# Performance work log

Measured on AMD Instinct MI355X. Metric: run time of the kernel, lower is better.

## Reference

```python
import jax, jax.numpy as jnp
import numpy as np

N = 50000
IN_DIM = 256
HID = 64
HEADS = 4
OUT_DIM = 64
NEG_SLOPE = 0.2


def gat_conv(x, src, dst, W, att_src, att_dst, bias, heads, out_ch):
    # x: [N, F_in]; src/dst: [E] (self-loops already appended)
    n = x.shape[0]
    h = (x @ W).reshape(n, heads, out_ch)                     # [N,H,C]
    a_s = jnp.sum(h * att_src, axis=-1)                       # [N,H]
    a_d = jnp.sum(h * att_dst, axis=-1)                       # [N,H]
    e = jax.nn.leaky_relu(a_s[src] + a_d[dst], NEG_SLOPE)     # [E,H]
    # segment softmax over destination neighborhoods
    m = jax.ops.segment_max(e, dst, num_segments=n)           # [N,H]
    m = jnp.where(jnp.isfinite(m), m, 0.0)
    ex = jnp.exp(e - m[dst])                                  # [E,H]
    denom = jax.ops.segment_sum(ex, dst, num_segments=n)      # [N,H]
    alpha = ex / (denom[dst] + 1e-16)                         # [E,H]
    msg = alpha[:, :, None] * h[src]                          # [E,H,C]
    out = jax.ops.segment_sum(msg, dst, num_segments=n)       # [N,H,C]
    return out.reshape(n, heads * out_ch) + bias


def setup_inputs() -> dict:
    key = jax.random.key(0)
    ks = jax.random.split(key, 10)
    glorot = lambda k, shape: jax.random.normal(k, shape, jnp.float32) * np.sqrt(2.0 / (shape[0] + shape[-1]))
    x = jax.random.normal(ks[0], (N, IN_DIM), jnp.float32)
    edge_index = jax.random.randint(ks[1], (2, 800000), 0, N, jnp.int64)
    W1 = glorot(ks[2], (IN_DIM, HEADS * HID))
    att_src1 = glorot(ks[3], (HEADS, HID))
    att_dst1 = glorot(ks[4], (HEADS, HID))
    b1 = jnp.zeros((HEADS * HID,), jnp.float32)
    W2 = glorot(ks[5], (HEADS * HID, OUT_DIM))
    att_src2 = glorot(ks[6], (1, OUT_DIM))
    att_dst2 = glorot(ks[7], (1, OUT_DIM))
    b2 = jnp.zeros((OUT_DIM,), jnp.float32)
    return {"x": x, "edge_index": edge_index, "W1": W1, "att_src1": att_src1,
            "att_dst1": att_dst1, "b1": b1, "W2": W2, "att_src2": att_src2,
            "att_dst2": att_dst2, "b2": b2}


def reference(x, edge_index, W1, att_src1, att_dst1, b1, W2, att_src2, att_dst2, b2):
    # add self loops (PyG GATConv default)
    loops = jnp.arange(N, dtype=edge_index.dtype)
    src = jnp.concatenate([edge_index[0], loops])
    dst = jnp.concatenate([edge_index[1], loops])
    h = gat_conv(x, src, dst, W1, att_src1, att_dst1, b1, HEADS, HID)
    h = jax.nn.elu(h)
    out = gat_conv(h, src, dst, W2, att_src2, att_dst2, b2, 1, OUT_DIM)
    return out
```

## Files before the change

### kernel.cpp

```cpp
#include <hip/hip_runtime.h>
#include <math.h>

#define N_NODES 50000
#define E_RAW   800000
#define E_TOT   850000
#define NEG_SLOPE 0.2f
#define NBC 196

typedef __attribute__((ext_vector_type(8))) short short8;
typedef __attribute__((ext_vector_type(4))) float f32x4;

__device__ __forceinline__ float lrelu(float v) {
    return v >= 0.f ? v : NEG_SLOPE * v;
}
__device__ __forceinline__ unsigned short f2bf(float f) {
    union { float f; unsigned u; } v; v.f = f;
    unsigned r = v.u + 0x7FFF + ((v.u >> 16) & 1);
    return (unsigned short)(r >> 16);
}
__device__ __forceinline__ float bf2f(unsigned short h) {
    union { unsigned u; float f; } v; v.u = ((unsigned)h) << 16;
    return v.f;
}
__device__ __forceinline__ int C1(int p) { return (p & 15) * 16 + (p >> 4); }
__device__ __forceinline__ int C2(int p) { return (p & 3) * 16 + (p >> 2); }

__global__ __launch_bounds__(256) void k_hist(
    const int* __restrict__ dst, int* __restrict__ counts)
{
    int e = blockIdx.x * 256 + threadIdx.x;
    if (e >= E_TOT) return;
    int d = (e < E_RAW) ? dst[e] : e - E_RAW;
    atomicAdd(&counts[d], 1);
}

__global__ __launch_bounds__(256) void k_scan1(
    const int* __restrict__ counts, int* __restrict__ off, int* __restrict__ bsum)
{
    __shared__ int sh[256];
    int t = threadIdx.x, i = blockIdx.x * 256 + t;
    int c = (i < N_NODES) ? counts[i] : 0;
    sh[t] = c; __syncthreads();
    for (int ofs = 1; ofs < 256; ofs <<= 1) {
        int v = (t >= ofs) ? sh[t - ofs] : 0;
        __syncthreads(); sh[t] += v; __syncthreads();
    }
    if (i < N_NODES) off[i] = sh[t] - c;
    if (t == 255) bsum[blockIdx.x] = sh[255];
}

__global__ __launch_bounds__(256) void k_scan2(int* __restrict__ bsum)
{
    __shared__ int sh[256];
    int t = threadIdx.x;
    int c = (t < NBC) ? bsum[t] : 0;
    sh[t] = c; __syncthreads();
    for (int ofs = 1; ofs < 256; ofs <<= 1) {
        int v = (t >= ofs) ? sh[t - ofs] : 0;
        __syncthreads(); sh[t] += v; __syncthreads();
    }
    if (t < NBC) bsum[t] = sh[t] - c;
}

__global__ __launch_bounds__(256) void k_scan3(
    int* __restrict__ off, const int* __restrict__ bsum)
{
    int i = blockIdx.x * 256 + threadIdx.x;
    if (i < N_NODES) off[i] += bsum[blockIdx.x];
    if (i == 0) off[N_NODES] = E_TOT;
}

__global__ __launch_bounds__(256) void k_scatter(
    const int* __restrict__ src, const int* __restrict__ dst,
    const int* __restrict__ off, int* __restrict__ cursor,
    int* __restrict__ esrc)
{
    int e = blockIdx.x * 256 + threadIdx.x;
    if (e >= E_TOT) return;
    int s, d;
    if (e < E_RAW) { s = src[e]; d = dst[e]; } else { s = e - E_RAW; d = s; }
    int pos = off[d] + atomicAdd(&cursor[d], 1);
    esrc[pos] = s;
}

__global__ __launch_bounds__(256) void k_prepw1(
    const float* __restrict__ W1, unsigned short* __restrict__ Wf1)
{
    int idx = blockIdx.x * 256 + threadIdx.x;
    int lane = idx & 63, kb = (idx >> 6) & 7, nb = idx >> 9;
    int c = nb * 16 + (lane & 15);
    int k0 = kb * 32 + ((lane >> 4) & 3) * 8;
    short8 pk;
#pragma unroll
    for (int j = 0; j < 8; ++j)
        pk[j] = (short)f2bf(W1[(k0 + j) * 256 + c]);
    *(short8*)&Wf1[idx * 8] = pk;
}

__global__ __launch_bounds__(256) void k_prepw2(
    const float* __restrict__ W2, unsigned short* __restrict__ Wf2)
{
    int idx = blockIdx.x * 256 + threadIdx.x;
    int lane = idx & 63, kb = (idx >> 6) & 7, nb = idx >> 9;
    int c = nb * 16 + (lane & 15);
    int k0 = kb * 32 + ((lane >> 4) & 3) * 8;
    short8 pk;
#pragma unroll
    for (int j = 0; j < 8; ++j) {
        int ktrue = C1(k0 + j);
        pk[j] = (short)f2bf(W2[ktrue * 64 + c]);
    }
    *(short8*)&Wf2[idx * 8] = pk;
}

__global__ __launch_bounds__(256) void k_gemm1(
    const float* __restrict__ x, const unsigned short* __restrict__ Wf1,
    const float* __restrict__ att_src, const float* __restrict__ att_dst,
    unsigned short* __restrict__ h1b, float* __restrict__ as1, float* __restrict__ ad1)
{
    const int t = threadIdx.x;
    const int lane = t & 63;
    const int w = t >> 6;
    const int rbase = blockIdx.x * 16;
    const int q  = lane & 15;
    const int kg = lane >> 4;
    const int rowA = rbase + q;

    f32x4 acc[4];
#pragma unroll
    for (int nb = 0; nb < 4; ++nb) acc[nb] = (f32x4){0.f, 0.f, 0.f, 0.f};

    short8 b[2][4];
    float4 a0, a1, a0n, a1n;
    {
        const float* ap = &x[rowA * 256 + kg * 8];
        a0 = *(const float4*)ap;
        a1 = *(const float4*)(ap + 4);
#pragma unroll
        for (int nb = 0; nb < 4; ++nb)
            b[0][nb] = *(const short8*)&Wf1[(((w * 4 + nb) * 8 + 0) * 64 + lane) * 8];
    }
#pragma unroll
    for (int kb = 0; kb < 8; ++kb) {
        if (kb < 7) {
            const float* ap = &x[rowA * 256 + (kb + 1) * 32 + kg * 8];
            a0n = *(const float4*)ap;
            a1n = *(const float4*)(ap + 4);
#pragma unroll
            for (int nb = 0; nb < 4; ++nb)
                b[(kb + 1) & 1][nb] =
                    *(const short8*)&Wf1[(((w * 4 + nb) * 8 + kb + 1) * 64 + lane) * 8];
        }
        short8 af;
        af[0] = (short)f2bf(a0.x); af[1] = (short)f2bf(a0.y);
        af[2] = (short)f2bf(a0.z); af[3] = (short)f2bf(a0.w);
        af[4] = (short)f2bf(a1.x); af[5] = (short)f2bf(a1.y);
        af[6] = (short)f2bf(a1.z); af[7] = (short)f2bf(a1.w);
#pragma unroll
        for (int nb = 0; nb < 4; ++nb)
            acc[nb] = __builtin_amdgcn_mfma_f32_16x16x32_bf16(af, b[kb & 1][nb], acc[nb], 0, 0, 0);
        if (kb < 7) { a0 = a0n; a1 = a1n; }
    }

#pragma unroll
    for (int reg = 0; reg < 4; ++reg) {
        int n = rbase + kg * 4 + reg;
        ushort4 pk;
        pk.x = f2bf(acc[0][reg]); pk.y = f2bf(acc[1][reg]);
        pk.z = f2bf(acc[2][reg]); pk.w = f2bf(acc[3][reg]);
        *(ushort4*)&h1b[n * 256 + q * 16 + w * 4] = pk;
    }
    float asv[4], adv[4];
#pragma unroll
    for (int nb = 0; nb < 4; ++nb) {
        int col = (w * 4 + nb) * 16 + q;
        asv[nb] = att_src[col];
        adv[nb] = att_dst[col];
    }
#pragma unroll
    for (int reg = 0; reg < 4; ++reg) {
        float s = acc[0][reg]*asv[0] + acc[1][reg]*asv[1] + acc[2][reg]*asv[2] + acc[3][reg]*asv[3];
        float d = acc[0][reg]*adv[0] + acc[1][reg]*adv[1] + acc[2][reg]*adv[2] + acc[3][reg]*adv[3];
#pragma unroll
        for (int ofs = 1; ofs < 16; ofs <<= 1) {
            s += __shfl_xor(s, ofs);
            d += __shfl_xor(d, ofs);
        }
        if (q == 0) {
            int n = rbase + kg * 4 + reg;
            as1[n * 4 + w] = s;
            ad1[n * 4 + w] = d;
        }
    }
}

__global__ __launch_bounds__(256) void k_gather1(
    const int* __restrict__ esrc, const int* __restrict__ off,
    const float* __restrict__ as1, const float* __restrict__ ad1,
    const unsigned short* __restrict__ h1b, const float* __restrict__ b1,
    unsigned short* __restrict__ hmid)
{
    int d    = (blockIdx.x * 256 + threadIdx.x) >> 6;
    int lane = threadIdx.x & 63;
    if (d >= N_NODES) return;
    const int head = lane & 3;
    const float adv = ad1[d * 4 + head];
    const int e0 = off[d], e1 = off[d + 1];
    float4 acc = make_float4(0.f, 0.f, 0.f, 0.f);
    float dn = 0.f;
    int e = e0;
    for (; e + 3 < e1; e += 4) {
        int s0 = esrc[e], s1 = esrc[e + 1], s2 = esrc[e + 2], s3 = esrc[e + 3];
        float w0 = __expf(lrelu(as1[s0 * 4 + head] + adv));
        float w1 = __expf(lrelu(as1[s1 * 4 + head] + adv));
        float w2 = __expf(lrelu(as1[s2 * 4 + head] + adv));
        float w3 = __expf(lrelu(as1[s3 * 4 + head] + adv));
        ushort4 u0 = *(const ushort4*)&h1b[s0 * 256 + lane * 4];
        ushort4 u1 = *(const ushort4*)&h1b[s1 * 256 + lane * 4];
        ushort4 u2 = *(const ushort4*)&h1b[s2 * 256 + lane * 4];
        ushort4 u3 = *(const ushort4*)&h1b[s3 * 256 + lane * 4];
        dn += (w0 + w1) + (w2 + w3);
        acc.x = fmaf(w0, bf2f(u0.x), fmaf(w1, bf2f(u1.x), fmaf(w2, bf2f(u2.x), fmaf(w3, bf2f(u3.x), acc.x))));
        acc.y = fmaf(w0, bf2f(u0.y), fmaf(w1, bf2f(u1.y), fmaf(w2, bf2f(u2.y), fmaf(w3, bf2f(u3.y), acc.y))));
        acc.z = fmaf(w0, bf2f(u0.z), fmaf(w1, bf2f(u1.z), fmaf(w2, bf2f(u2.z), fmaf(w3, bf2f(u3.z), acc.z))));
        acc.w = fmaf(w0, bf2f(u0.w), fmaf(w1, bf2f(u1.w), fmaf(w2, bf2f(u2.w), fmaf(w3, bf2f(u3.w), acc.w))));
    }
    for (; e < e1; ++e) {
        int s0 = esrc[e];
        float w0 = __expf(lrelu(as1[s0 * 4 + head] + adv));
        ushort4 u0 = *(const ushort4*)&h1b[s0 * 256 + lane * 4];
        dn += w0;
        acc.x = fmaf(w0, bf2f(u0.x), acc.x);
        acc.y = fmaf(w0, bf2f(u0.y), acc.y);
        acc.z = fmaf(w0, bf2f(u0.z), acc.z);
        acc.w = fmaf(w0, bf2f(u0.w), acc.w);
    }
    const float inv = 1.f / (dn + 1e-16f);
    float o[4] = {acc.x, acc.y, acc.z, acc.w};
    ushort4 pk;
    unsigned short* pko = (unsigned short*)&pk;
#pragma unroll
    for (int i = 0; i < 4; ++i) {
        float v = o[i] * inv + b1[C1(lane * 4 + i)];
        v = v > 0.f ? v : expm1f(v);
        pko[i] = f2bf(v);
    }
    *(ushort4*)&hmid[d * 256 + lane * 4] = pk;
}

__global__ __launch_bounds__(256) void k_gemm2(
    const unsigned short* __restrict__ hmid, const unsigned short* __restrict__ Wf2,
    const float* __restrict__ att_src, const float* __restrict__ att_dst,
    unsigned short* __restrict__ h2b, float* __restrict__ as2, float* __restrict__ ad2)
{
    const int t = threadIdx.x;
    const int lane = t & 63;
    const int w = t >> 6;
    const int rbase = blockIdx.x * 64 + w * 16;
    const int q  = lane & 15;
    const int kg = lane >> 4;
    const int rowA = rbase + q;
    const int rA = rowA < N_NODES ? rowA : N_NODES - 1;

    f32x4 acc[4];
#pragma unroll
    for (int nb = 0; nb < 4; ++nb) acc[nb] = (f32x4){0.f, 0.f, 0.f, 0.f};

    short8 b[2][4];
    short8 af, afn;
    af = *(const short8*)&hmid[rA * 256 + kg * 8];
#pragma unroll
    for (int nb = 0; nb < 4; ++nb)
        b[0][nb] = *(const short8*)&Wf2[((nb * 8 + 0) * 64 + lane) * 8];
#pragma unroll
    for (int kb = 0; kb < 8; ++kb) {
        if (kb < 7) {
            afn = *(const short8*)&hmid[rA * 256 + (kb + 1) * 32 + kg * 8];
#pragma unroll
            for (int nb = 0; nb < 4; ++nb)
                b[(kb + 1) & 1][nb] = *(const short8*)&Wf2[((nb * 8 + kb + 1) * 64 + lane) * 8];
        }
#pragma unroll
        for (int nb = 0; nb < 4; ++nb)
            acc[nb] = __builtin_amdgcn_mfma_f32_16x16x32_bf16(af, b[kb & 1][nb], acc[nb], 0, 0, 0);
        if (kb < 7) af = afn;
    }

    float asv[4], adv[4];
#pragma unroll
    for (int nb = 0; nb < 4; ++nb) {
        int col = nb * 16 + q;
        asv[nb] = att_src[col];
        adv[nb] = att_dst[col];
    }
#pragma unroll
    for (int reg = 0; reg < 4; ++reg) {
        int n = rbase + kg * 4 + reg;
        bool ok = n < N_NODES;
        if (ok) {
            ushort4 pk;
            pk.x = f2bf(acc[0][reg]); pk.y = f2bf(acc[1][reg]);
            pk.z = f2bf(acc[2][reg]); pk.w = f2bf(acc[3][reg]);
            *(ushort4*)&h2b[n * 64 + q * 4] = pk;
        }
        float s = acc[0][reg]*asv[0] + acc[1][reg]*asv[1] + acc[2][reg]*asv[2] + acc[3][reg]*asv[3];
        float d = acc[0][reg]*adv[0] + acc[1][reg]*adv[1] + acc[2][reg]*adv[2] + acc[3][reg]*adv[3];
#pragma unroll
        for (int ofs = 1; ofs < 16; ofs <<= 1) {
            s += __shfl_xor(s, ofs);
            d += __shfl_xor(d, ofs);
        }
        if (ok && q == 0) { as2[n] = s; ad2[n] = d; }
    }
}

__global__ __launch_bounds__(256) void k_gather2(
    const int* __restrict__ esrc, const int* __restrict__ off,
    const float* __restrict__ as2, const float* __restrict__ ad2,
    const unsigned short* __restrict__ h2b, const float* __restrict__ b2,
    float* __restrict__ out)
{
    int d    = (blockIdx.x * 256 + threadIdx.x) >> 6;
    int lane = threadIdx.x & 63;
    if (d >= N_NODES) return;
    const float adv = ad2[d];
    const int e0 = off[d], e1 = off[d + 1];
    float acc = 0.f, dn = 0.f;
    int e = e0;
    for (; e + 3 < e1; e += 4) {
        int s0 = esrc[e], s1 = esrc[e + 1], s2 = esrc[e + 2], s3 = esrc[e + 3];
        float w0 = __expf(lrelu(as2[s0] + adv));
        float w1 = __expf(lrelu(as2[s1] + adv));
        float w2 = __expf(lrelu(as2[s2] + adv));
        float w3 = __expf(lrelu(as2[s3] + adv));
        float v0 = bf2f(h2b[s0 * 64 + lane]);
        float v1 = bf2f(h2b[s1 * 64 + lane]);
        float v2 = bf2f(h2b[s2 * 64 + lane]);
        float v3 = bf2f(h2b[s3 * 64 + lane]);
        dn += (w0 + w1) + (w2 + w3);
        acc = fmaf(w0, v0, fmaf(w1, v1, fmaf(w2, v2, fmaf(w3, v3, acc))));
    }
    for (; e < e1; ++e) {
        int s0 = esrc[e];
        float w0 = __expf(lrelu(as2[s0] + adv));
        float v0 = bf2f(h2b[s0 * 64 + lane]);
        dn += w0;
        acc = fmaf(w0, v0, acc);
    }
    int col = C2(lane);
    out[d * 64 + col] = acc / (dn + 1e-16f) + b2[col];
}

extern "C" void kernel_launch(void* const* d_in, const int* in_sizes, int n_in,
                              void* d_out, int out_size, void* d_ws, size_t ws_size,
                              hipStream_t stream)
{
    const float* x        = (const float*)d_in[0];
    const int*   ei       = (const int*)d_in[1];
    const float* W1       = (const float*)d_in[2];
    const float* att_src1 = (const float*)d_in[3];
    const float* att_dst1 = (const float*)d_in[4];
    const float* b1       = (const float*)d_in[5];
    const float* W2       = (const float*)d_in[6];
    const float* att_src2 = (const float*)d_in[7];
    const float* att_dst2 = (const float*)d_in[8];
    const float* b2       = (const float*)d_in[9];
    const int* src = ei;
    const int* dst = ei + E_RAW;
    float* out = (float*)d_out;

    char* ws = (char*)d_ws;
    int*            counts = (int*)(ws + 0);
    int*            cursor = (int*)(ws + 200000);
    int*            off    = (int*)(ws + 400000);
    int*            bsum   = (int*)(ws + 600064);
    float*          as1    = (float*)(ws + 600896);
    float*          ad1    = (float*)(ws + 1400896);
    float*          as2    = (float*)(ws + 2200896);
    float*          ad2    = (float*)(ws + 2400896);
    int*            esrc   = (int*)(ws + 2600896);
    unsigned short* Wf1    = (unsigned short*)(ws + 6000896);
    unsigned short* Wf2    = (unsigned short*)(ws + 6131968);
    unsigned short* h1b    = (unsigned short*)(ws + 6164736);
    unsigned short* h2b    = (unsigned short*)(ws + 6164736);
    unsigned short* hmid   = (unsigned short*)(ws + 31764736);

    hipMemsetAsync(ws, 0, 400000, stream);

    const int EB = (E_TOT + 255) / 256;
    k_prepw1 <<<32, 256, 0, stream>>>(W1, Wf1);
    k_prepw2 <<<8, 256, 0, stream>>>(W2, Wf2);
    k_hist   <<<EB, 256, 0, stream>>>(dst, counts);
    k_scan1  <<<NBC, 256, 0, stream>>>(counts, off, bsum);
    k_scan2  <<<1, 256, 0, stream>>>(bsum);
    k_scan3  <<<NBC, 256, 0, stream>>>(off, bsum);
    k_scatter<<<EB, 256, 0, stream>>>(src, dst, off, cursor, esrc);

    k_gemm1  <<<3125, 256, 0, stream>>>(x, Wf1, att_src1, att_dst1, h1b, as1, ad1);
    k_gather1<<<12500, 256, 0, stream>>>(esrc, off, as1, ad1, h1b, b1, hmid);
    k_gemm2  <<<782, 256, 0, stream>>>(hmid, Wf2, att_src2, att_dst2, h2b, as2, ad2);
    k_gather2<<<12500, 256, 0, stream>>>(esrc, off, as2, ad2, h2b, b2, out);
}
```

Before: 265.5 us.

## Split attention softmax into separate kernels and column-partition gathers across XCDs

```diff
diff --git a/kernel.cpp b/kernel.cpp
--- a/kernel.cpp
+++ b/kernel.cpp
@@ -22,8 +22,6 @@
     union { unsigned u; float f; } v; v.u = ((unsigned)h) << 16;
     return v.f;
 }
-__device__ __forceinline__ int C1(int p) { return (p & 15) * 16 + (p >> 4); }
-__device__ __forceinline__ int C2(int p) { return (p & 3) * 16 + (p >> 2); }
 
 __global__ __launch_bounds__(256) void k_hist(
     const int* __restrict__ dst, int* __restrict__ counts)
@@ -106,10 +104,8 @@
     int k0 = kb * 32 + ((lane >> 4) & 3) * 8;
     short8 pk;
 #pragma unroll
-    for (int j = 0; j < 8; ++j) {
-        int ktrue = C1(k0 + j);
-        pk[j] = (short)f2bf(W2[ktrue * 64 + c]);
-    }
+    for (int j = 0; j < 8; ++j)
+        pk[j] = (short)f2bf(W2[(k0 + j) * 64 + c]);
     *(short8*)&Wf2[idx * 8] = pk;
 }
 
@@ -165,10 +161,9 @@
 #pragma unroll
     for (int reg = 0; reg < 4; ++reg) {
         int n = rbase + kg * 4 + reg;
-        ushort4 pk;
-        pk.x = f2bf(acc[0][reg]); pk.y = f2bf(acc[1][reg]);
-        pk.z = f2bf(acc[2][reg]); pk.w = f2bf(acc[3][reg]);
-        *(ushort4*)&h1b[n * 256 + q * 16 + w * 4] = pk;
+#pragma unroll
+        for (int nb = 0; nb < 4; ++nb)
+            h1b[n * 256 + (w * 4 + nb) * 16 + q] = f2bf(acc[nb][reg]);
     }
     float asv[4], adv[4];
 #pragma unroll
@@ -194,58 +189,81 @@
     }
 }
 
-__global__ __launch_bounds__(256) void k_gather1(
+__global__ __launch_bounds__(256) void k_alpha1(
     const int* __restrict__ esrc, const int* __restrict__ off,
     const float* __restrict__ as1, const float* __restrict__ ad1,
-    const unsigned short* __restrict__ h1b, const float* __restrict__ b1,
-    unsigned short* __restrict__ hmid)
+    unsigned short* __restrict__ aw1)
 {
     int d    = (blockIdx.x * 256 + threadIdx.x) >> 6;
     int lane = threadIdx.x & 63;
     if (d >= N_NODES) return;
     const int head = lane & 3;
+    const int ei   = lane >> 2;
     const float adv = ad1[d * 4 + head];
     const int e0 = off[d], e1 = off[d + 1];
-    float4 acc = make_float4(0.f, 0.f, 0.f, 0.f);
     float dn = 0.f;
-    int e = e0;
-    for (; e + 3 < e1; e += 4) {
-        int s0 = esrc[e], s1 = esrc[e + 1], s2 = esrc[e + 2], s3 = esrc[e + 3];
-        float w0 = __expf(lrelu(as1[s0 * 4 + head] + adv));
-        float w1 = __expf(lrelu(as1[s1 * 4 + head] + adv));
-        float w2 = __expf(lrelu(as1[s2 * 4 + head] + adv));
-        float w3 = __expf(lrelu(as1[s3 * 4 + head] + adv));
-        ushort4 u0 = *(const ushort4*)&h1b[s0 * 256 + lane * 4];
-        ushort4 u1 = *(const ushort4*)&h1b[s1 * 256 + lane * 4];
-        ushort4 u2 = *(const ushort4*)&h1b[s2 * 256 + lane * 4];
-        ushort4 u3 = *(const ushort4*)&h1b[s3 * 256 + lane * 4];
-        dn += (w0 + w1) + (w2 + w3);
-        acc.x = fmaf(w0, bf2f(u0.x), fmaf(w1, bf2f(u1.x), fmaf(w2, bf2f(u2.x), fmaf(w3, bf2f(u3.x), acc.x))));
-        acc.y = fmaf(w0, bf2f(u0.y), fmaf(w1, bf2f(u1.y), fmaf(w2, bf2f(u2.y), fmaf(w3, bf2f(u3.y), acc.y))));
-        acc.z = fmaf(w0, bf2f(u0.z), fmaf(w1, bf2f(u1.z), fmaf(w2, bf2f(u2.z), fmaf(w3, bf2f(u3.z), acc.z))));
-        acc.w = fmaf(w0, bf2f(u0.w), fmaf(w1, bf2f(u1.w), fmaf(w2, bf2f(u2.w), fmaf(w3, bf2f(u3.w), acc.w))));
-    }
-    for (; e < e1; ++e) {
-        int s0 = esrc[e];
-        float w0 = __expf(lrelu(as1[s0 * 4 + head] + adv));
-        ushort4 u0 = *(const ushort4*)&h1b[s0 * 256 + lane * 4];
-        dn += w0;
-        acc.x = fmaf(w0, bf2f(u0.x), acc.x);
-        acc.y = fmaf(w0, bf2f(u0.y), acc.y);
-        acc.z = fmaf(w0, bf2f(u0.z), acc.z);
-        acc.w = fmaf(w0, bf2f(u0.w), acc.w);
-    }
+    for (int e = e0 + ei; e < e1; e += 16) {
+        int s = esrc[e];
+        float wv = __expf(lrelu(as1[s * 4 + head] + adv));
+        unsigned short r = f2bf(wv);
+        dn += bf2f(r);
+        aw1[e * 4 + head] = r;
+    }
+#pragma unroll
+    for (int ofs = 4; ofs < 64; ofs <<= 1) dn += __shfl_xor(dn, ofs);
     const float inv = 1.f / (dn + 1e-16f);
-    float o[4] = {acc.x, acc.y, acc.z, acc.w};
-    ushort4 pk;
-    unsigned short* pko = (unsigned short*)&pk;
-#pragma unroll
-    for (int i = 0; i < 4; ++i) {
-        float v = o[i] * inv + b1[C1(lane * 4 + i)];
-        v = v > 0.f ? v : expm1f(v);
-        pko[i] = f2bf(v);
-    }
-    *(ushort4*)&hmid[d * 256 + lane * 4] = pk;
+    for (int e = e0 + ei; e < e1; e += 16) {
+        float wv = bf2f(aw1[e * 4 + head]);
+        aw1[e * 4 + head] = f2bf(wv * inv);
+    }
+}
+
+__global__ __launch_bounds__(256) void k_gather1(
+    const int* __restrict__ esrc, const int* __restrict__ off,
+    const unsigned short* __restrict__ aw1,
+    const unsigned short* __restrict__ h1b, const float* __restrict__ b1,
+    unsigned short* __restrict__ hmid)
+{
+    const int bid = blockIdx.x;
+    const int cg  = bid & 7;
+    const int t = threadIdx.x;
+    const int w = t >> 6;
+    const int lane = t & 63;
+    const int d = (bid >> 3) * 4 + w;
+    const int k  = lane & 15;
+    const int ep = lane >> 4;
+    const int head = cg >> 1;
+    const int e0 = off[d], e1 = off[d + 1];
+    const unsigned short* hb = h1b + cg * 32 + k * 2;
+    float a0 = 0.f, a1 = 0.f;
+    int e = e0 + ep;
+    for (; e + 4 < e1; e += 8) {
+        int sA = esrc[e], sB = esrc[e + 4];
+        float wA = bf2f(aw1[e * 4 + head]);
+        float wB = bf2f(aw1[(e + 4) * 4 + head]);
+        unsigned uA = *(const unsigned*)(hb + sA * 256);
+        unsigned uB = *(const unsigned*)(hb + sB * 256);
+        a0 = fmaf(wA, bf2f((unsigned short)uA), fmaf(wB, bf2f((unsigned short)uB), a0));
+        a1 = fmaf(wA, bf2f((unsigned short)(uA >> 16)), fmaf(wB, bf2f((unsigned short)(uB >> 16)), a1));
+    }
+    if (e < e1) {
+        int sA = esrc[e];
+        float wA = bf2f(aw1[e * 4 + head]);
+        unsigned uA = *(const unsigned*)(hb + sA * 256);
+        a0 = fmaf(wA, bf2f((unsigned short)uA), a0);
+        a1 = fmaf(wA, bf2f((unsigned short)(uA >> 16)), a1);
+    }
+    a0 += __shfl_xor(a0, 16); a0 += __shfl_xor(a0, 32);
+    a1 += __shfl_xor(a1, 16); a1 += __shfl_xor(a1, 32);
+    if (ep == 0) {
+        int col = cg * 32 + k * 2;
+        float v0 = a0 + b1[col];
+        float v1 = a1 + b1[col + 1];
+        v0 = v0 > 0.f ? v0 : expm1f(v0);
+        v1 = v1 > 0.f ? v1 : expm1f(v1);
+        unsigned pk = (unsigned)f2bf(v0) | ((unsigned)f2bf(v1) << 16);
+        *(unsigned*)&hmid[d * 256 + col] = pk;
+    }
 }
 
 __global__ __launch_bounds__(256) void k_gemm2(
@@ -298,10 +316,9 @@
         int n = rbase + kg * 4 + reg;
         bool ok = n < N_NODES;
         if (ok) {
-            ushort4 pk;
-            pk.x = f2bf(acc[0][reg]); pk.y = f2bf(acc[1][reg]);
-            pk.z = f2bf(acc[2][reg]); pk.w = f2bf(acc[3][reg]);
-            *(ushort4*)&h2b[n * 64 + q * 4] = pk;
+#pragma unroll
+            for (int nb = 0; nb < 4; ++nb)
+                h2b[n * 64 + nb * 16 + q] = f2bf(acc[nb][reg]);
         }
         float s = acc[0][reg]*asv[0] + acc[1][reg]*asv[1] + acc[2][reg]*asv[2] + acc[3][reg]*asv[3];
         float d = acc[0][reg]*adv[0] + acc[1][reg]*adv[1] + acc[2][reg]*adv[2] + acc[3][reg]*adv[3];
@@ -314,41 +331,77 @@
     }
 }
 
-__global__ __launch_bounds__(256) void k_gather2(
+__global__ __launch_bounds__(256) void k_alpha2(
     const int* __restrict__ esrc, const int* __restrict__ off,
     const float* __restrict__ as2, const float* __restrict__ ad2,
-    const unsigned short* __restrict__ h2b, const float* __restrict__ b2,
-    float* __restrict__ out)
+    unsigned short* __restrict__ aw2)
 {
     int d    = (blockIdx.x * 256 + threadIdx.x) >> 6;
     int lane = threadIdx.x & 63;
     if (d >= N_NODES) return;
     const float adv = ad2[d];
     const int e0 = off[d], e1 = off[d + 1];
-    float acc = 0.f, dn = 0.f;
-    int e = e0;
-    for (; e + 3 < e1; e += 4) {
-        int s0 = esrc[e], s1 = esrc[e + 1], s2 = esrc[e + 2], s3 = esrc[e + 3];
-        float w0 = __expf(lrelu(as2[s0] + adv));
-        float w1 = __expf(lrelu(as2[s1] + adv));
-        float w2 = __expf(lrelu(as2[s2] + adv));
-        float w3 = __expf(lrelu(as2[s3] + adv));
-        float v0 = bf2f(h2b[s0 * 64 + lane]);
-        float v1 = bf2f(h2b[s1 * 64 + lane]);
-        float v2 = bf2f(h2b[s2 * 64 + lane]);
-        float v3 = bf2f(h2b[s3 * 64 + lane]);
-        dn += (w0 + w1) + (w2 + w3);
-        acc = fmaf(w0, v0, fmaf(w1, v1, fmaf(w2, v2, fmaf(w3, v3, acc))));
-    }
-    for (; e < e1; ++e) {
-        int s0 = esrc[e];
-        float w0 = __expf(lrelu(as2[s0] + adv));
-        float v0 = bf2f(h2b[s0 * 64 + lane]);
-        dn += w0;
-        acc = fmaf(w0, v0, acc);
-    }
-    int col = C2(lane);
-    out[d * 64 + col] = acc / (dn + 1e-16f) + b2[col];
+    float dn = 0.f;
+    for (int e = e0 + lane; e < e1; e += 64) {
+        int s = esrc[e];
+        float wv = __expf(lrelu(as2[s] + adv));
+        unsigned short r = f2bf(wv);
+        dn += bf2f(r);
+        aw2[e] = r;
+    }
+#pragma unroll
+    for (int ofs = 1; ofs < 64; ofs <<= 1) dn += __shfl_xor(dn, ofs);
+    const float inv = 1.f / (dn + 1e-16f);
+    for (int e = e0 + lane; e < e1; e += 64) {
+        aw2[e] = f2bf(bf2f(aw2[e]) * inv);
+    }
+}
+
+__global__ __launch_bounds__(256) void k_gather2(
+    const int* __restrict__ esrc, const int* __restrict__ off,
+    const unsigned short* __restrict__ aw2,
+    const unsigned short* __restrict__ h2b, const float* __restrict__ b2,
+    float* __restrict__ out)
+{
+    const int bid = blockIdx.x;
+    const int xcd = bid & 7;
+    const int cg  = xcd >> 2;
+    const int sub = xcd & 3;
+    const int t = threadIdx.x;
+    const int w = t >> 6;
+    const int lane = t & 63;
+    const int d = ((bid >> 3) * 4 + sub) * 4 + w;
+    const int k  = lane & 15;
+    const int ep = lane >> 4;
+    const int e0 = off[d], e1 = off[d + 1];
+    const unsigned short* hb = h2b + cg * 32 + k * 2;
+    float a0 = 0.f, a1 = 0.f;
+    int e = e0 + ep;
+    for (; e + 4 < e1; e += 8) {
+        int sA = esrc[e], sB = esrc[e + 4];
+        float wA = bf2f(aw2[e]);
+        float wB = bf2f(aw2[e + 4]);
+        unsigned uA = *(const unsigned*)(hb + sA * 64);
+        unsigned uB = *(const unsigned*)(hb + sB * 64);
+        a0 = fmaf(wA, bf2f((unsigned short)uA), fmaf(wB, bf2f((unsigned short)uB), a0));
+        a1 = fmaf(wA, bf2f((unsigned short)(uA >> 16)), fmaf(wB, bf2f((unsigned short)(uB >> 16)), a1));
+    }
+    if (e < e1) {
+        int sA = esrc[e];
+        float wA = bf2f(aw2[e]);
+        unsigned uA = *(const unsigned*)(hb + sA * 64);
+        a0 = fmaf(wA, bf2f((unsigned short)uA), a0);
+        a1 = fmaf(wA, bf2f((unsigned short)(uA >> 16)), a1);
+    }
+    a0 += __shfl_xor(a0, 16); a0 += __shfl_xor(a0, 32);
+    a1 += __shfl_xor(a1, 16); a1 += __shfl_xor(a1, 32);
+    if (ep == 0) {
+        int col = cg * 32 + k * 2;
+        float2 o;
+        o.x = a0 + b2[col];
+        o.y = a1 + b2[col + 1];
+        *(float2*)&out[d * 64 + col] = o;
+    }
 }
 
 extern "C" void kernel_launch(void* const* d_in, const int* in_sizes, int n_in,
@@ -381,9 +434,11 @@
     int*            esrc   = (int*)(ws + 2600896);
     unsigned short* Wf1    = (unsigned short*)(ws + 6000896);
     unsigned short* Wf2    = (unsigned short*)(ws + 6131968);
-    unsigned short* h1b    = (unsigned short*)(ws + 6164736);
-    unsigned short* h2b    = (unsigned short*)(ws + 6164736);
-    unsigned short* hmid   = (unsigned short*)(ws + 31764736);
+    unsigned short* aw1    = (unsigned short*)(ws + 6164736);
+    unsigned short* aw2    = (unsigned short*)(ws + 12964736);
+    unsigned short* h1b    = (unsigned short*)(ws + 14664736);
+    unsigned short* h2b    = (unsigned short*)(ws + 14664736);
+    unsigned short* hmid   = (unsigned short*)(ws + 40264736);
 
     hipMemsetAsync(ws, 0, 400000, stream);
 
@@ -397,7 +452,9 @@
     k_scatter<<<EB, 256, 0, stream>>>(src, dst, off, cursor, esrc);
 
     k_gemm1  <<<3125, 256, 0, stream>>>(x, Wf1, att_src1, att_dst1, h1b, as1, ad1);
-    k_gather1<<<12500, 256, 0, stream>>>(esrc, off, as1, ad1, h1b, b1, hmid);
+    k_alpha1 <<<12500, 256, 0, stream>>>(esrc, off, as1, ad1, aw1);
+    k_gather1<<<100000, 256, 0, stream>>>(esrc, off, aw1, h1b, b1, hmid);
     k_gemm2  <<<782, 256, 0, stream>>>(hmid, Wf2, att_src2, att_dst2, h2b, as2, ad2);
-    k_gather2<<<12500, 256, 0, stream>>>(esrc, off, as2, ad2, h2b, b2, out);
-}
+    k_alpha2 <<<12500, 256, 0, stream>>>(esrc, off, as2, ad2, aw2);
+    k_gather2<<<25000, 256, 0, stream>>>(esrc, off, aw2, h2b, b2, out);
+}
```

Result: slower. 411.1 us (+54.9%).

## Compress edge sources to 16-bit and widen per-lane gathers in aggregation kernels

Applied to the files above, without the earlier changes.

```diff
diff --git a/kernel.cpp b/kernel.cpp
--- a/kernel.cpp
+++ b/kernel.cpp
@@ -73,44 +73,41 @@
 __global__ __launch_bounds__(256) void k_scatter(
     const int* __restrict__ src, const int* __restrict__ dst,
     const int* __restrict__ off, int* __restrict__ cursor,
-    int* __restrict__ esrc)
+    unsigned short* __restrict__ esrc)
 {
     int e = blockIdx.x * 256 + threadIdx.x;
     if (e >= E_TOT) return;
     int s, d;
     if (e < E_RAW) { s = src[e]; d = dst[e]; } else { s = e - E_RAW; d = s; }
     int pos = off[d] + atomicAdd(&cursor[d], 1);
-    esrc[pos] = s;
-}
-
-__global__ __launch_bounds__(256) void k_prepw1(
-    const float* __restrict__ W1, unsigned short* __restrict__ Wf1)
+    esrc[pos] = (unsigned short)s;
+}
+
+__global__ __launch_bounds__(256) void k_prepw(
+    const float* __restrict__ W1, const float* __restrict__ W2,
+    unsigned short* __restrict__ Wf1, unsigned short* __restrict__ Wf2)
 {
     int idx = blockIdx.x * 256 + threadIdx.x;
-    int lane = idx & 63, kb = (idx >> 6) & 7, nb = idx >> 9;
-    int c = nb * 16 + (lane & 15);
-    int k0 = kb * 32 + ((lane >> 4) & 3) * 8;
-    short8 pk;
-#pragma unroll
-    for (int j = 0; j < 8; ++j)
-        pk[j] = (short)f2bf(W1[(k0 + j) * 256 + c]);
-    *(short8*)&Wf1[idx * 8] = pk;
-}
-
-__global__ __launch_bounds__(256) void k_prepw2(
-    const float* __restrict__ W2, unsigned short* __restrict__ Wf2)
-{
-    int idx = blockIdx.x * 256 + threadIdx.x;
-    int lane = idx & 63, kb = (idx >> 6) & 7, nb = idx >> 9;
-    int c = nb * 16 + (lane & 15);
-    int k0 = kb * 32 + ((lane >> 4) & 3) * 8;
-    short8 pk;
-#pragma unroll
-    for (int j = 0; j < 8; ++j) {
-        int ktrue = C1(k0 + j);
-        pk[j] = (short)f2bf(W2[ktrue * 64 + c]);
-    }
-    *(short8*)&Wf2[idx * 8] = pk;
+    if (idx < 8192) {
+        int lane = idx & 63, kb = (idx >> 6) & 7, nb = idx >> 9;
+        int c = nb * 16 + (lane & 15);
+        int k0 = kb * 32 + ((lane >> 4) & 3) * 8;
+        short8 pk;
+#pragma unroll
+        for (int j = 0; j < 8; ++j)
+            pk[j] = (short)f2bf(W1[(k0 + j) * 256 + c]);
+        *(short8*)&Wf1[idx * 8] = pk;
+    } else if (idx < 10240) {
+        int i2 = idx - 8192;
+        int lane = i2 & 63, kb = (i2 >> 6) & 7, nb = i2 >> 9;
+        int c = nb * 16 + (lane & 15);
+        int k0 = kb * 32 + ((lane >> 4) & 3) * 8;
+        short8 pk;
+#pragma unroll
+        for (int j = 0; j < 8; ++j)
+            pk[j] = (short)f2bf(W2[C1(k0 + j) * 64 + c]);
+        *(short8*)&Wf2[i2 * 8] = pk;
+    }
 }
 
 __global__ __launch_bounds__(256) void k_gemm1(
@@ -195,57 +192,83 @@
 }
 
 __global__ __launch_bounds__(256) void k_gather1(
-    const int* __restrict__ esrc, const int* __restrict__ off,
+    const unsigned short* __restrict__ esrc, const int* __restrict__ off,
     const float* __restrict__ as1, const float* __restrict__ ad1,
     const unsigned short* __restrict__ h1b, const float* __restrict__ b1,
     unsigned short* __restrict__ hmid)
 {
-    int d    = (blockIdx.x * 256 + threadIdx.x) >> 6;
-    int lane = threadIdx.x & 63;
-    if (d >= N_NODES) return;
-    const int head = lane & 3;
-    const float adv = ad1[d * 4 + head];
+    const int t = threadIdx.x;
+    const int w = t >> 6;
+    const int lane = t & 63;
+    const int h = lane >> 5;
+    const int j = lane & 31;
+    const int d = blockIdx.x * 8 + w * 2 + h;
+    const int hA = 2 * (j & 1);
+    const float2 advv = *(const float2*)&ad1[d * 4 + hA];
     const int e0 = off[d], e1 = off[d + 1];
-    float4 acc = make_float4(0.f, 0.f, 0.f, 0.f);
-    float dn = 0.f;
+    const unsigned short* hb = h1b + j * 8;
+
+    float acc[8];
+#pragma unroll
+    for (int i = 0; i < 8; ++i) acc[i] = 0.f;
+    float dnA = 0.f, dnB = 0.f;
+
     int e = e0;
     for (; e + 3 < e1; e += 4) {
         int s0 = esrc[e], s1 = esrc[e + 1], s2 = esrc[e + 2], s3 = esrc[e + 3];
-        float w0 = __expf(lrelu(as1[s0 * 4 + head] + adv));
-        float w1 = __expf(lrelu(as1[s1 * 4 + head] + adv));
-        float w2 = __expf(lrelu(as1[s2 * 4 + head] + adv));
-        float w3 = __expf(lrelu(as1[s3 * 4 + head] + adv));
-        ushort4 u0 = *(const ushort4*)&h1b[s0 * 256 + lane * 4];
-        ushort4 u1 = *(const ushort4*)&h1b[s1 * 256 + lane * 4];
-        ushort4 u2 = *(const ushort4*)&h1b[s2 * 256 + lane * 4];
-        ushort4 u3 = *(const ushort4*)&h1b[s3 * 256 + lane * 4];
-        dn += (w0 + w1) + (w2 + w3);
-        acc.x = fmaf(w0, bf2f(u0.x), fmaf(w1, bf2f(u1.x), fmaf(w2, bf2f(u2.x), fmaf(w3, bf2f(u3.x), acc.x))));
-        acc.y = fmaf(w0, bf2f(u0.y), fmaf(w1, bf2f(u1.y), fmaf(w2, bf2f(u2.y), fmaf(w3, bf2f(u3.y), acc.y))));
-        acc.z = fmaf(w0, bf2f(u0.z), fmaf(w1, bf2f(u1.z), fmaf(w2, bf2f(u2.z), fmaf(w3, bf2f(u3.z), acc.z))));
-        acc.w = fmaf(w0, bf2f(u0.w), fmaf(w1, bf2f(u1.w), fmaf(w2, bf2f(u2.w), fmaf(w3, bf2f(u3.w), acc.w))));
+        float2 q0 = *(const float2*)&as1[s0 * 4 + hA];
+        float2 q1 = *(const float2*)&as1[s1 * 4 + hA];
+        float2 q2 = *(const float2*)&as1[s2 * 4 + hA];
+        float2 q3 = *(const float2*)&as1[s3 * 4 + hA];
+        short8 u0 = *(const short8*)(hb + s0 * 256);
+        short8 u1 = *(const short8*)(hb + s1 * 256);
+        short8 u2 = *(const short8*)(hb + s2 * 256);
+        short8 u3 = *(const short8*)(hb + s3 * 256);
+        float wA0 = __expf(lrelu(q0.x + advv.x));
+        float wB0 = __expf(lrelu(q0.y + advv.y));
+        float wA1 = __expf(lrelu(q1.x + advv.x));
+        float wB1 = __expf(lrelu(q1.y + advv.y));
+        float wA2 = __expf(lrelu(q2.x + advv.x));
+        float wB2 = __expf(lrelu(q2.y + advv.y));
+        float wA3 = __expf(lrelu(q3.x + advv.x));
+        float wB3 = __expf(lrelu(q3.y + advv.y));
+        dnA += (wA0 + wA1) + (wA2 + wA3);
+        dnB += (wB0 + wB1) + (wB2 + wB3);
+#pragma unroll
+        for (int i = 0; i < 4; ++i) {
+            acc[i] = fmaf(wA0, bf2f((unsigned short)u0[i]),
+                     fmaf(wA1, bf2f((unsigned short)u1[i]),
+                     fmaf(wA2, bf2f((unsigned short)u2[i]),
+                     fmaf(wA3, bf2f((unsigned short)u3[i]), acc[i]))));
+            acc[4 + i] = fmaf(wB0, bf2f((unsigned short)u0[4 + i]),
+                         fmaf(wB1, bf2f((unsigned short)u1[4 + i]),
+                         fmaf(wB2, bf2f((unsigned short)u2[4 + i]),
+                         fmaf(wB3, bf2f((unsigned short)u3[4 + i]), acc[4 + i]))));
+        }
     }
     for (; e < e1; ++e) {
         int s0 = esrc[e];
-        float w0 = __expf(lrelu(as1[s0 * 4 + head] + adv));
-        ushort4 u0 = *(const ushort4*)&h1b[s0 * 256 + lane * 4];
-        dn += w0;
-        acc.x = fmaf(w0, bf2f(u0.x), acc.x);
-        acc.y = fmaf(w0, bf2f(u0.y), acc.y);
-        acc.z = fmaf(w0, bf2f(u0.z), acc.z);
-        acc.w = fmaf(w0, bf2f(u0.w), acc.w);
-    }
-    const float inv = 1.f / (dn + 1e-16f);
-    float o[4] = {acc.x, acc.y, acc.z, acc.w};
-    ushort4 pk;
-    unsigned short* pko = (unsigned short*)&pk;
-#pragma unroll
-    for (int i = 0; i < 4; ++i) {
-        float v = o[i] * inv + b1[C1(lane * 4 + i)];
+        float2 q0 = *(const float2*)&as1[s0 * 4 + hA];
+        short8 u0 = *(const short8*)(hb + s0 * 256);
+        float wA0 = __expf(lrelu(q0.x + advv.x));
+        float wB0 = __expf(lrelu(q0.y + advv.y));
+        dnA += wA0; dnB += wB0;
+#pragma unroll
+        for (int i = 0; i < 4; ++i) {
+            acc[i]     = fmaf(wA0, bf2f((unsigned short)u0[i]), acc[i]);
+            acc[4 + i] = fmaf(wB0, bf2f((unsigned short)u0[4 + i]), acc[4 + i]);
+        }
+    }
+    const float invA = 1.f / (dnA + 1e-16f);
+    const float invB = 1.f / (dnB + 1e-16f);
+    short8 pk;
+#pragma unroll
+    for (int i = 0; i < 8; ++i) {
+        float v = acc[i] * (i < 4 ? invA : invB) + b1[C1(j * 8 + i)];
         v = v > 0.f ? v : expm1f(v);
-        pko[i] = f2bf(v);
-    }
-    *(ushort4*)&hmid[d * 256 + lane * 4] = pk;
+        pk[i] = (short)f2bf(v);
+    }
+    *(short8*)&hmid[d * 256 + j * 8] = pk;
 }
 
 __global__ __launch_bounds__(256) void k_gemm2(
@@ -315,17 +338,23 @@
 }
 
 __global__ __launch_bounds__(256) void k_gather2(
-    const int* __restrict__ esrc, const int* __restrict__ off,
+    const unsigned short* __restrict__ esrc, const int* __restrict__ off,
     const float* __restrict__ as2, const float* __restrict__ ad2,
     const unsigned short* __restrict__ h2b, const float* __restrict__ b2,
     float* __restrict__ out)
 {
-    int d    = (blockIdx.x * 256 + threadIdx.x) >> 6;
-    int lane = threadIdx.x & 63;
-    if (d >= N_NODES) return;
+    const int t = threadIdx.x;
+    const int w = t >> 6;
+    const int lane = t & 63;
+    const int g  = lane >> 4;
+    const int j2 = lane & 15;
+    const int d = blockIdx.x * 16 + w * 4 + g;
     const float adv = ad2[d];
     const int e0 = off[d], e1 = off[d + 1];
-    float acc = 0.f, dn = 0.f;
+    const unsigned short* hb = h2b + j2 * 4;
+
+    float acc[4] = {0.f, 0.f, 0.f, 0.f};
+    float dn = 0.f;
     int e = e0;
     for (; e + 3 < e1; e += 4) {
         int s0 = esrc[e], s1 = esrc[e + 1], s2 = esrc[e + 2], s3 = esrc[e + 3];
@@ -333,22 +362,32 @@
         float w1 = __expf(lrelu(as2[s1] + adv));
         float w2 = __expf(lrelu(as2[s2] + adv));
         float w3 = __expf(lrelu(as2[s3] + adv));
-        float v0 = bf2f(h2b[s0 * 64 + lane]);
-        float v1 = bf2f(h2b[s1 * 64 + lane]);
-        float v2 = bf2f(h2b[s2 * 64 + lane]);
-        float v3 = bf2f(h2b[s3 * 64 + lane]);
+        ushort4 u0 = *(const ushort4*)(hb + s0 * 64);
+        ushort4 u1 = *(const ushort4*)(hb + s1 * 64);
+        ushort4 u2 = *(const ushort4*)(hb + s2 * 64);
+        ushort4 u3 = *(const ushort4*)(hb + s3 * 64);
         dn += (w0 + w1) + (w2 + w3);
-        acc = fmaf(w0, v0, fmaf(w1, v1, fmaf(w2, v2, fmaf(w3, v3, acc))));
+        acc[0] = fmaf(w0, bf2f(u0.x), fmaf(w1, bf2f(u1.x), fmaf(w2, bf2f(u2.x), fmaf(w3, bf2f(u3.x), acc[0]))));
+        acc[1] = fmaf(w0, bf2f(u0.y), fmaf(w1, bf2f(u1.y), fmaf(w2, bf2f(u2.y), fmaf(w3, bf2f(u3.y), acc[1]))));
+        acc[2] = fmaf(w0, bf2f(u0.z), fmaf(w1, bf2f(u1.z), fmaf(w2, bf2f(u2.z), fmaf(w3, bf2f(u3.z), acc[2]))));
+        acc[3] = fmaf(w0, bf2f(u0.w), fmaf(w1, bf2f(u1.w), fmaf(w2, bf2f(u2.w), fmaf(w3, bf2f(u3.w), acc[3]))));
     }
     for (; e < e1; ++e) {
         int s0 = esrc[e];
         float w0 = __expf(lrelu(as2[s0] + adv));
-        float v0 = bf2f(h2b[s0 * 64 + lane]);
+        ushort4 u0 = *(const ushort4*)(hb + s0 * 64);
         dn += w0;
-        acc = fmaf(w0, v0, acc);
-    }
-    int col = C2(lane);
-    out[d * 64 + col] = acc / (dn + 1e-16f) + b2[col];
+        acc[0] = fmaf(w0, bf2f(u0.x), acc[0]);
+        acc[1] = fmaf(w0, bf2f(u0.y), acc[1]);
+        acc[2] = fmaf(w0, bf2f(u0.z), acc[2]);
+        acc[3] = fmaf(w0, bf2f(u0.w), acc[3]);
+    }
+    const float inv = 1.f / (dn + 1e-16f);
+#pragma unroll
+    for (int i = 0; i < 4; ++i) {
+        int col = i * 16 + j2;
+        out[d * 64 + col] = acc[i] * inv + b2[col];
+    }
 }
 
 extern "C" void kernel_launch(void* const* d_in, const int* in_sizes, int n_in,
@@ -378,18 +417,17 @@
     float*          ad1    = (float*)(ws + 1400896);
     float*          as2    = (float*)(ws + 2200896);
     float*          ad2    = (float*)(ws + 2400896);
-    int*            esrc   = (int*)(ws + 2600896);
-    unsigned short* Wf1    = (unsigned short*)(ws + 6000896);
-    unsigned short* Wf2    = (unsigned short*)(ws + 6131968);
-    unsigned short* h1b    = (unsigned short*)(ws + 6164736);
-    unsigned short* h2b    = (unsigned short*)(ws + 6164736);
-    unsigned short* hmid   = (unsigned short*)(ws + 31764736);
+    unsigned short* esrc   = (unsigned short*)(ws + 2600896);
+    unsigned short* Wf1    = (unsigned short*)(ws + 4300896);
+    unsigned short* Wf2    = (unsigned short*)(ws + 4431968);
+    unsigned short* h1b    = (unsigned short*)(ws + 4464736);
+    unsigned short* h2b    = (unsigned short*)(ws + 4464736);
+    unsigned short* hmid   = (unsigned short*)(ws + 30064736);
 
     hipMemsetAsync(ws, 0, 400000, stream);
 
     const int EB = (E_TOT + 255) / 256;
-    k_prepw1 <<<32, 256, 0, stream>>>(W1, Wf1);
-    k_prepw2 <<<8, 256, 0, stream>>>(W2, Wf2);
+    k_prepw  <<<40, 256, 0, stream>>>(W1, W2, Wf1, Wf2);
     k_hist   <<<EB, 256, 0, stream>>>(dst, counts);
     k_scan1  <<<NBC, 256, 0, stream>>>(counts, off, bsum);
     k_scan2  <<<1, 256, 0, stream>>>(bsum);
@@ -397,7 +435,7 @@
     k_scatter<<<EB, 256, 0, stream>>>(src, dst, off, cursor, esrc);
 
     k_gemm1  <<<3125, 256, 0, stream>>>(x, Wf1, att_src1, att_dst1, h1b, as1, ad1);
-    k_gather1<<<12500, 256, 0, stream>>>(esrc, off, as1, ad1, h1b, b1, hmid);
+    k_gather1<<<6250, 256, 0, stream>>>(esrc, off, as1, ad1, h1b, b1, hmid);
     k_gemm2  <<<782, 256, 0, stream>>>(hmid, Wf2, att_src2, att_dst2, h2b, as2, ad2);
-    k_gather2<<<12500, 256, 0, stream>>>(esrc, off, as2, ad2, h2b, b2, out);
-}
+    k_gather2<<<3125, 256, 0, stream>>>(esrc, off, as2, ad2, h2b, b2, out);
+}
```

Result: faster. 255.2 us (-3.9%).

## Precompute layer-1 edge weights in scatter, fuse prep kernels, vectorize gather2

Applied to the files above, without the earlier changes.

```diff
diff --git a/kernel.cpp b/kernel.cpp
--- a/kernel.cpp
+++ b/kernel.cpp
@@ -25,13 +25,36 @@
 __device__ __forceinline__ int C1(int p) { return (p & 15) * 16 + (p >> 4); }
 __device__ __forceinline__ int C2(int p) { return (p & 3) * 16 + (p >> 2); }
 
-__global__ __launch_bounds__(256) void k_hist(
-    const int* __restrict__ dst, int* __restrict__ counts)
-{
-    int e = blockIdx.x * 256 + threadIdx.x;
-    if (e >= E_TOT) return;
-    int d = (e < E_RAW) ? dst[e] : e - E_RAW;
-    atomicAdd(&counts[d], 1);
+__global__ __launch_bounds__(256) void k_prep_hist(
+    const int* __restrict__ dst, int* __restrict__ counts,
+    const float* __restrict__ W1, const float* __restrict__ W2,
+    unsigned short* __restrict__ Wf1, unsigned short* __restrict__ Wf2)
+{
+    int idx = blockIdx.x * 256 + threadIdx.x;
+    if (idx < 8192) {
+        int lane = idx & 63, kb = (idx >> 6) & 7, nb = idx >> 9;
+        int c = nb * 16 + (lane & 15);
+        int k0 = kb * 32 + ((lane >> 4) & 3) * 8;
+        short8 pk;
+#pragma unroll
+        for (int j = 0; j < 8; ++j)
+            pk[j] = (short)f2bf(W1[(k0 + j) * 256 + c]);
+        *(short8*)&Wf1[idx * 8] = pk;
+    } else if (idx < 10240) {
+        int i2 = idx - 8192;
+        int lane = i2 & 63, kb = (i2 >> 6) & 7, nb = i2 >> 9;
+        int c = nb * 16 + (lane & 15);
+        int k0 = kb * 32 + ((lane >> 4) & 3) * 8;
+        short8 pk;
+#pragma unroll
+        for (int j = 0; j < 8; ++j)
+            pk[j] = (short)f2bf(W2[C1(k0 + j) * 64 + c]);
+        *(short8*)&Wf2[i2 * 8] = pk;
+    }
+    if (idx < E_TOT) {
+        int d = (idx < E_RAW) ? dst[idx] : idx - E_RAW;
+        atomicAdd(&counts[d], 1);
+    }
 }
 
 __global__ __launch_bounds__(256) void k_scan1(
@@ -73,44 +96,23 @@
 __global__ __launch_bounds__(256) void k_scatter(
     const int* __restrict__ src, const int* __restrict__ dst,
     const int* __restrict__ off, int* __restrict__ cursor,
-    int* __restrict__ esrc)
+    const float* __restrict__ as1, const float* __restrict__ ad1,
+    unsigned short* __restrict__ esrc, float* __restrict__ aw1)
 {
     int e = blockIdx.x * 256 + threadIdx.x;
     if (e >= E_TOT) return;
     int s, d;
     if (e < E_RAW) { s = src[e]; d = dst[e]; } else { s = e - E_RAW; d = s; }
     int pos = off[d] + atomicAdd(&cursor[d], 1);
-    esrc[pos] = s;
-}
-
-__global__ __launch_bounds__(256) void k_prepw1(
-    const float* __restrict__ W1, unsigned short* __restrict__ Wf1)
-{
-    int idx = blockIdx.x * 256 + threadIdx.x;
-    int lane = idx & 63, kb = (idx >> 6) & 7, nb = idx >> 9;
-    int c = nb * 16 + (lane & 15);
-    int k0 = kb * 32 + ((lane >> 4) & 3) * 8;
-    short8 pk;
-#pragma unroll
-    for (int j = 0; j < 8; ++j)
-        pk[j] = (short)f2bf(W1[(k0 + j) * 256 + c]);
-    *(short8*)&Wf1[idx * 8] = pk;
-}
-
-__global__ __launch_bounds__(256) void k_prepw2(
-    const float* __restrict__ W2, unsigned short* __restrict__ Wf2)
-{
-    int idx = blockIdx.x * 256 + threadIdx.x;
-    int lane = idx & 63, kb = (idx >> 6) & 7, nb = idx >> 9;
-    int c = nb * 16 + (lane & 15);
-    int k0 = kb * 32 + ((lane >> 4) & 3) * 8;
-    short8 pk;
-#pragma unroll
-    for (int j = 0; j < 8; ++j) {
-        int ktrue = C1(k0 + j);
-        pk[j] = (short)f2bf(W2[ktrue * 64 + c]);
-    }
-    *(short8*)&Wf2[idx * 8] = pk;
+    esrc[pos] = (unsigned short)s;
+    float4 A = *(const float4*)&as1[s * 4];
+    float4 B = *(const float4*)&ad1[d * 4];
+    float4 w;
+    w.x = __expf(lrelu(A.x + B.x));
+    w.y = __expf(lrelu(A.y + B.y));
+    w.z = __expf(lrelu(A.z + B.z));
+    w.w = __expf(lrelu(A.w + B.w));
+    *(float4*)&aw1[pos * 4] = w;
 }
 
 __global__ __launch_bounds__(256) void k_gemm1(
@@ -195,26 +197,24 @@
 }
 
 __global__ __launch_bounds__(256) void k_gather1(
-    const int* __restrict__ esrc, const int* __restrict__ off,
-    const float* __restrict__ as1, const float* __restrict__ ad1,
+    const unsigned short* __restrict__ esrc, const int* __restrict__ off,
+    const float* __restrict__ aw1,
     const unsigned short* __restrict__ h1b, const float* __restrict__ b1,
     unsigned short* __restrict__ hmid)
 {
     int d    = (blockIdx.x * 256 + threadIdx.x) >> 6;
     int lane = threadIdx.x & 63;
-    if (d >= N_NODES) return;
     const int head = lane & 3;
-    const float adv = ad1[d * 4 + head];
     const int e0 = off[d], e1 = off[d + 1];
     float4 acc = make_float4(0.f, 0.f, 0.f, 0.f);
     float dn = 0.f;
     int e = e0;
     for (; e + 3 < e1; e += 4) {
         int s0 = esrc[e], s1 = esrc[e + 1], s2 = esrc[e + 2], s3 = esrc[e + 3];
-        float w0 = __expf(lrelu(as1[s0 * 4 + head] + adv));
-        float w1 = __expf(lrelu(as1[s1 * 4 + head] + adv));
-        float w2 = __expf(lrelu(as1[s2 * 4 + head] + adv));
-        float w3 = __expf(lrelu(as1[s3 * 4 + head] + adv));
+        float w0 = aw1[(e + 0) * 4 + head];
+        float w1 = aw1[(e + 1) * 4 + head];
+        float w2 = aw1[(e + 2) * 4 + head];
+        float w3 = aw1[(e + 3) * 4 + head];
         ushort4 u0 = *(const ushort4*)&h1b[s0 * 256 + lane * 4];
         ushort4 u1 = *(const ushort4*)&h1b[s1 * 256 + lane * 4];
         ushort4 u2 = *(const ushort4*)&h1b[s2 * 256 + lane * 4];
@@ -227,7 +227,7 @@
     }
     for (; e < e1; ++e) {
         int s0 = esrc[e];
-        float w0 = __expf(lrelu(as1[s0 * 4 + head] + adv));
+        float w0 = aw1[e * 4 + head];
         ushort4 u0 = *(const ushort4*)&h1b[s0 * 256 + lane * 4];
         dn += w0;
         acc.x = fmaf(w0, bf2f(u0.x), acc.x);
@@ -315,17 +315,23 @@
 }
 
 __global__ __launch_bounds__(256) void k_gather2(
-    const int* __restrict__ esrc, const int* __restrict__ off,
+    const unsigned short* __restrict__ esrc, const int* __restrict__ off,
     const float* __restrict__ as2, const float* __restrict__ ad2,
     const unsigned short* __restrict__ h2b, const float* __restrict__ b2,
     float* __restrict__ out)
 {
-    int d    = (blockIdx.x * 256 + threadIdx.x) >> 6;
-    int lane = threadIdx.x & 63;
-    if (d >= N_NODES) return;
+    const int t = threadIdx.x;
+    const int w = t >> 6;
+    const int lane = t & 63;
+    const int g  = lane >> 4;
+    const int j2 = lane & 15;
+    const int d = blockIdx.x * 16 + w * 4 + g;
     const float adv = ad2[d];
     const int e0 = off[d], e1 = off[d + 1];
-    float acc = 0.f, dn = 0.f;
+    const unsigned short* hb = h2b + j2 * 4;
+
+    float acc[4] = {0.f, 0.f, 0.f, 0.f};
+    float dn = 0.f;
     int e = e0;
     for (; e + 3 < e1; e += 4) {
         int s0 = esrc[e], s1 = esrc[e + 1], s2 = esrc[e + 2], s3 = esrc[e + 3];
@@ -333,22 +339,32 @@
         float w1 = __expf(lrelu(as2[s1] + adv));
         float w2 = __expf(lrelu(as2[s2] + adv));
         float w3 = __expf(lrelu(as2[s3] + adv));
-        float v0 = bf2f(h2b[s0 * 64 + lane]);
-        float v1 = bf2f(h2b[s1 * 64 + lane]);
-        float v2 = bf2f(h2b[s2 * 64 + lane]);
-        float v3 = bf2f(h2b[s3 * 64 + lane]);
+        ushort4 u0 = *(const ushort4*)(hb + s0 * 64);
+        ushort4 u1 = *(const ushort4*)(hb + s1 * 64);
+        ushort4 u2 = *(const ushort4*)(hb + s2 * 64);
+        ushort4 u3 = *(const ushort4*)(hb + s3 * 64);
         dn += (w0 + w1) + (w2 + w3);
-        acc = fmaf(w0, v0, fmaf(w1, v1, fmaf(w2, v2, fmaf(w3, v3, acc))));
+        acc[0] = fmaf(w0, bf2f(u0.x), fmaf(w1, bf2f(u1.x), fmaf(w2, bf2f(u2.x), fmaf(w3, bf2f(u3.x), acc[0]))));
+        acc[1] = fmaf(w0, bf2f(u0.y), fmaf(w1, bf2f(u1.y), fmaf(w2, bf2f(u2.y), fmaf(w3, bf2f(u3.y), acc[1]))));
+        acc[2] = fmaf(w0, bf2f(u0.z), fmaf(w1, bf2f(u1.z), fmaf(w2, bf2f(u2.z), fmaf(w3, bf2f(u3.z), acc[2]))));
+        acc[3] = fmaf(w0, bf2f(u0.w), fmaf(w1, bf2f(u1.w), fmaf(w2, bf2f(u2.w), fmaf(w3, bf2f(u3.w), acc[3]))));
     }
     for (; e < e1; ++e) {
         int s0 = esrc[e];
         float w0 = __expf(lrelu(as2[s0] + adv));
-        float v0 = bf2f(h2b[s0 * 64 + lane]);
+        ushort4 u0 = *(const ushort4*)(hb + s0 * 64);
         dn += w0;
-        acc = fmaf(w0, v0, acc);
-    }
-    int col = C2(lane);
-    out[d * 64 + col] = acc / (dn + 1e-16f) + b2[col];
+        acc[0] = fmaf(w0, bf2f(u0.x), acc[0]);
+        acc[1] = fmaf(w0, bf2f(u0.y), acc[1]);
+        acc[2] = fmaf(w0, bf2f(u0.z), acc[2]);
+        acc[3] = fmaf(w0, bf2f(u0.w), acc[3]);
+    }
+    const float inv = 1.f / (dn + 1e-16f);
+#pragma unroll
+    for (int i = 0; i < 4; ++i) {
+        int col = i * 16 + j2;
+        out[d * 64 + col] = acc[i] * inv + b2[col];
+    }
 }
 
 extern "C" void kernel_launch(void* const* d_in, const int* in_sizes, int n_in,
@@ -378,26 +394,24 @@
     float*          ad1    = (float*)(ws + 1400896);
     float*          as2    = (float*)(ws + 2200896);
     float*          ad2    = (float*)(ws + 2400896);
-    int*            esrc   = (int*)(ws + 2600896);
-    unsigned short* Wf1    = (unsigned short*)(ws + 6000896);
-    unsigned short* Wf2    = (unsigned short*)(ws + 6131968);
-    unsigned short* h1b    = (unsigned short*)(ws + 6164736);
-    unsigned short* h2b    = (unsigned short*)(ws + 6164736);
-    unsigned short* hmid   = (unsigned short*)(ws + 31764736);
+    unsigned short* esrc   = (unsigned short*)(ws + 2600896);
+    unsigned short* Wf1    = (unsigned short*)(ws + 4300896);
+    unsigned short* Wf2    = (unsigned short*)(ws + 4431968);
+    float*          aw1    = (float*)(ws + 4464736);
+    unsigned short* h1b    = (unsigned short*)(ws + 18064736);
+    unsigned short* h2b    = (unsigned short*)(ws + 18064736);
+    unsigned short* hmid   = (unsigned short*)(ws + 43664736);
 
     hipMemsetAsync(ws, 0, 400000, stream);
 
     const int EB = (E_TOT + 255) / 256;
-    k_prepw1 <<<32, 256, 0, stream>>>(W1, Wf1);
-    k_prepw2 <<<8, 256, 0, stream>>>(W2, Wf2);
-    k_hist   <<<EB, 256, 0, stream>>>(dst, counts);
+    k_prep_hist<<<EB, 256, 0, stream>>>(dst, counts, W1, W2, Wf1, Wf2);
     k_scan1  <<<NBC, 256, 0, stream>>>(counts, off, bsum);
     k_scan2  <<<1, 256, 0, stream>>>(bsum);
     k_scan3  <<<NBC, 256, 0, stream>>>(off, bsum);
-    k_scatter<<<EB, 256, 0, stream>>>(src, dst, off, cursor, esrc);
-
     k_gemm1  <<<3125, 256, 0, stream>>>(x, Wf1, att_src1, att_dst1, h1b, as1, ad1);
-    k_gather1<<<12500, 256, 0, stream>>>(esrc, off, as1, ad1, h1b, b1, hmid);
+    k_scatter<<<EB, 256, 0, stream>>>(src, dst, off, cursor, as1, ad1, esrc, aw1);
+    k_gather1<<<12500, 256, 0, stream>>>(esrc, off, aw1, h1b, b1, hmid);
     k_gemm2  <<<782, 256, 0, stream>>>(hmid, Wf2, att_src2, att_dst2, h2b, as2, ad2);
-    k_gather2<<<12500, 256, 0, stream>>>(esrc, off, as2, ad2, h2b, b2, out);
-}
+    k_gather2<<<3125, 256, 0, stream>>>(esrc, off, as2, ad2, h2b, b2, out);
+}
```

After: 249.1 us. 1.07x faster.
